# Optimization experiments

Hardware: AMD Instinct MI355X
Metric: run time of the kernel (lower is better)

The kernel has to match this reference:

```python
import jax, jax.numpy as jnp
import numpy as np

B, C_IN, N = 4, 128, 4096
E = 131072           # nnz edges in the sparse adjacency
C_OUT = 128          # module out_channels
C_CONV = C_OUT - 1   # add_counts=True steals one channel for degree counts


def setup_inputs() -> dict:
    key = jax.random.key(0)
    kx, ki, kj, kw, kb = jax.random.split(key, 5)
    x = jax.random.normal(kx, (B, C_IN, N), dtype=jnp.float32)
    # edge list (i, j) for each nonzero of the sparse adjacency
    idx_i = jax.random.randint(ki, (E,), 0, N)
    idx_j = jax.random.randint(kj, (E,), 0, N)
    # Conv1d(in=C_IN, out=C_CONV, kernel_size=2, stride=2) weights
    W = jax.random.normal(kw, (C_CONV, C_IN, 2), dtype=jnp.float32) * 0.05
    b = jax.random.normal(kb, (C_CONV,), dtype=jnp.float32) * 0.05
    return {"x": x, "W": W, "b": b, "idx_i": idx_i, "idx_j": idx_j}


def reference(x, W, b, idx_i, idx_j):
    # _conv: x @ adj_pw.T is a gather of the two endpoints of every edge
    # (adj_pw row 2k selects node idx_i[k], row 2k+1 selects node idx_j[k]).
    # Conv1d(kernel=2, stride=2) then mixes the interleaved endpoint pair:
    #   pair[b,o,e] = sum_c W[o,c,0]*x[b,c,i_e] + W[o,c,1]*x[b,c,j_e] + b[o]
    xi = x[:, :, idx_i]                                   # [B, C, E]
    xj = x[:, :, idx_j]                                   # [B, C, E]
    pair = (jnp.einsum('oc,bce->boe', W[:, :, 0], xi)
            + jnp.einsum('oc,bce->boe', W[:, :, 1], xj)
            + b[None, :, None])                           # [B, C_CONV, E]
    # x @ adj_pw[::2, :] scatter-adds each edge's output to its first endpoint
    n = x.shape[2]
    y = jnp.zeros((x.shape[0], pair.shape[1], n), dtype=x.dtype)
    y = y.at[:, :, idx_i].add(pair)                       # [B, C_CONV, N]
    # adj_sum = adj.to_dense().sum(dim=0): in-degree over columns j
    deg = jnp.zeros((n,), dtype=x.dtype).at[idx_j].add(1.0)
    # normalize: divide by degree clamped to >= 1
    y = y / jnp.where(deg == 0, 1.0, deg)
    # add_counts: append raw degree as an extra channel
    counts = jnp.broadcast_to(deg[None, None, :], (y.shape[0], 1, n))
    return jnp.concatenate([y, counts], axis=1)           # [B, C_OUT, N]
```

## Files before the change

kernel.cpp:

```cpp
#include <hip/hip_runtime.h>
#include <cstdint>
#include <cstddef>

#define BATCH   4
#define CIN     128
#define NN      4096
#define EE      131072
#define CCONV   127
#define NBC     512
#define MAXDEG  128

typedef __attribute__((ext_vector_type(8))) short short8;
typedef __attribute__((ext_vector_type(8))) unsigned short ushort8;
typedef __attribute__((ext_vector_type(4))) float f32x4;

__device__ __forceinline__ unsigned short f2bf(float f) {
    unsigned int u = __float_as_uint(f);
    return (unsigned short)((u + 0x7FFFu + ((u >> 16) & 1u)) >> 16);
}
__device__ __forceinline__ float bf2f(unsigned short h) {
    return __uint_as_float((unsigned int)h << 16);
}

__global__ __launch_bounds__(256) void k_pre(const float* __restrict__ x,
                                             unsigned short* __restrict__ xT,
                                             const float* __restrict__ W,
                                             unsigned short* __restrict__ WTb,
                                             const int* __restrict__ idx_i,
                                             const int* __restrict__ idx_j,
                                             int* __restrict__ cursor,
                                             unsigned short* __restrict__ elist,
                                             int* __restrict__ deg) {
    const int bid = blockIdx.x;
    const int tid = threadIdx.x;
    if (bid < 2048) {
        __shared__ float tile[32][33];
        const int nb = bid & 127;
        const int cb = (bid >> 7) & 3;
        const int b  = bid >> 9;
        const int n0 = nb * 32, c0 = cb * 32;
        const int tx = tid & 31, ty = tid >> 5;
        const float* xb = x + (size_t)b * CIN * NN;
#pragma unroll
        for (int i = 0; i < 4; ++i)
            tile[ty + i * 8][tx] = xb[(size_t)(c0 + ty + i * 8) * NN + n0 + tx];
        __syncthreads();
#pragma unroll
        for (int i = 0; i < 4; ++i) {
            const int nl = ty + i * 8;
            xT[(size_t)(n0 + nl) * NBC + b * CIN + c0 + tx] = f2bf(tile[tx][nl]);
        }
    } else if (bid < 2560) {
        const int e  = (bid - 2048) * 256 + tid;
        const int ni = idx_i[e];
        const int nj = idx_j[e];
        const int pos = atomicAdd(&cursor[ni], 1);
        elist[(size_t)ni * MAXDEG + pos] = (unsigned short)nj;
        atomicAdd(&deg[nj], 1);
    } else {
        const int t = (bid - 2560) * 256 + tid;
        const int o = t >> 8;
        const int k = t & 255;
        float v = 0.0f;
        if (o < CCONV) v = W[((size_t)o * CIN + (k & 127)) * 2 + (k >> 7)];
        WTb[t] = f2bf(v);
    }
}

__global__ __launch_bounds__(256) void k_final(const unsigned short* __restrict__ xT,
                                               const unsigned short* __restrict__ WTb,
                                               const float* __restrict__ bias,
                                               const unsigned short* __restrict__ elist,
                                               const int* __restrict__ cnt_i,
                                               const int* __restrict__ deg,
                                               float* __restrict__ out) {
    __shared__ short Af[1024 * 8];
    __shared__ float cntf[32], invd[32], degf[32], biasf[128];
    __shared__ int   cnti[32];

    const int tid = threadIdx.x;
    const int b   = blockIdx.y;
    const int n0  = blockIdx.x * 32;

    if (tid < 32) {
        const int c = cnt_i[n0 + tid];
        const int d = deg[n0 + tid];
        cnti[tid] = c;
        cntf[tid] = (float)c;
        degf[tid] = (float)d;
        invd[tid] = (d == 0) ? 1.0f : 1.0f / (float)d;
    } else if (tid >= 64 && tid < 192) {
        const int o = tid - 64;
        biasf[o] = (o < CCONV) ? bias[o] : 0.0f;
    }
    __syncthreads();

    const int lane = tid & 63;
    const int w    = tid >> 6;

    {
        const int ns = lane >> 4;
        const int c0 = (lane & 15) * 8;
        const unsigned short* xb = xT + b * CIN + c0;
#pragma unroll
        for (int pg = 0; pg < 2; ++pg) {
            const int j  = w * 8 + pg * 4 + ns;
            const int dn = cnti[j];
            const unsigned short* erow = elist + (size_t)(n0 + j) * MAXDEG;
            float acc[8] = {0, 0, 0, 0, 0, 0, 0, 0};
            int k = 0;
            for (; k + 2 <= dn; k += 2) {
                const int nj0 = erow[k];
                const int nj1 = erow[k + 1];
                const ushort8 u0 = *(const ushort8*)(xb + (size_t)nj0 * NBC);
                const ushort8 u1 = *(const ushort8*)(xb + (size_t)nj1 * NBC);
#pragma unroll
                for (int q = 0; q < 8; ++q) acc[q] += bf2f(u0[q]) + bf2f(u1[q]);
            }
            if (k < dn) {
                const int nj = erow[k];
                const ushort8 u = *(const ushort8*)(xb + (size_t)nj * NBC);
#pragma unroll
                for (int q = 0; q < 8; ++q) acc[q] += bf2f(u[q]);
            }
            short8 p;
#pragma unroll
            for (int q = 0; q < 8; ++q) p[q] = (short)f2bf(acc[q]);
            const int kt   = 4 + (c0 >> 5);
            const int g    = (c0 >> 3) & 3;
            const int unit = ((j >> 4) * 8 + kt) * 64 + (j & 15) + 16 * g;
            *(short8*)&Af[unit * 8] = p;
        }
    }

#pragma unroll
    for (int it = 0; it < 2; ++it) {
        const int u  = tid + it * 256;
        const int L  = u & 63;
        const int kt = (u >> 6) & 3;
        const int mt = u >> 8;
        const int j  = mt * 16 + (L & 15);
        const int k0 = kt * 32 + (L >> 4) * 8;
        const short8 a = *(const short8*)(xT + (size_t)(n0 + j) * NBC + b * CIN + k0);
        const float sc = cntf[j];
        short8 p;
#pragma unroll
        for (int q = 0; q < 8; ++q)
            p[q] = (short)f2bf(bf2f((unsigned short)a[q]) * sc);
        *(short8*)&Af[((mt * 8 + kt) * 64 + L) * 8] = p;
    }
    __syncthreads();

    const int m = lane & 15;
    const int g = lane >> 4;

    f32x4 acc[2][2];
#pragma unroll
    for (int mt = 0; mt < 2; ++mt)
#pragma unroll
        for (int nt = 0; nt < 2; ++nt)
            acc[mt][nt] = (f32x4){0.0f, 0.0f, 0.0f, 0.0f};

    const unsigned short* B0 = WTb + (size_t)(w * 32 + m) * 256;
    const unsigned short* B1 = B0 + 16 * 256;

#pragma unroll
    for (int kt = 0; kt < 8; ++kt) {
        const int k0 = kt * 32 + g * 8;
        const short8 b0 = *(const short8*)(B0 + k0);
        const short8 b1 = *(const short8*)(B1 + k0);
        const short8 a0 = *(const short8*)&Af[((0 * 8 + kt) * 64 + lane) * 8];
        const short8 a1 = *(const short8*)&Af[((1 * 8 + kt) * 64 + lane) * 8];
        acc[0][0] = __builtin_amdgcn_mfma_f32_16x16x32_bf16(a0, b0, acc[0][0], 0, 0, 0);
        acc[0][1] = __builtin_amdgcn_mfma_f32_16x16x32_bf16(a0, b1, acc[0][1], 0, 0, 0);
        acc[1][0] = __builtin_amdgcn_mfma_f32_16x16x32_bf16(a1, b0, acc[1][0], 0, 0, 0);
        acc[1][1] = __builtin_amdgcn_mfma_f32_16x16x32_bf16(a1, b1, acc[1][1], 0, 0, 0);
    }

#pragma unroll
    for (int nt = 0; nt < 2; ++nt) {
        const int o = w * 32 + nt * 16 + m;
        if (o >= CCONV) continue;
        const float bo = biasf[o];
        float* orow = out + ((size_t)b * 128 + o) * NN + n0;
#pragma unroll
        for (int mt = 0; mt < 2; ++mt) {
            const int j0 = mt * 16 + g * 4;
            float4 r;
            r.x = (acc[mt][nt][0] + cntf[j0 + 0] * bo) * invd[j0 + 0];
            r.y = (acc[mt][nt][1] + cntf[j0 + 1] * bo) * invd[j0 + 1];
            r.z = (acc[mt][nt][2] + cntf[j0 + 2] * bo) * invd[j0 + 2];
            r.w = (acc[mt][nt][3] + cntf[j0 + 3] * bo) * invd[j0 + 3];
            *(float4*)(orow + j0) = r;
        }
    }
    if (tid < 32)
        out[((size_t)b * 128 + CCONV) * NN + n0 + tid] = degf[tid];
}

extern "C" void kernel_launch(void* const* d_in, const int* in_sizes, int n_in,
                              void* d_out, int out_size, void* d_ws, size_t ws_size,
                              hipStream_t stream) {
    const float* x    = (const float*)d_in[0];
    const float* W    = (const float*)d_in[1];
    const float* bias = (const float*)d_in[2];
    const int* idx_i  = (const int*)d_in[3];
    const int* idx_j  = (const int*)d_in[4];
    float* out = (float*)d_out;

    char* ws = (char*)d_ws;
    unsigned short* xT     = (unsigned short*)(ws);
    unsigned short* elist  = (unsigned short*)(ws + 4194304);
    unsigned short* WTb    = (unsigned short*)(ws + 5242880);
    int*            cursor = (int*)(ws + 5308416);
    int*            deg    = (int*)(ws + 5324800);

    hipMemsetAsync(cursor, 0, 32768, stream);

    k_pre<<<2688, 256, 0, stream>>>(x, xT, W, WTb, idx_i, idx_j, cursor, elist, deg);
    k_final<<<dim3(NN / 32, BATCH), 256, 0, stream>>>(xT, WTb, bias, elist, cursor, deg, out);
}
```

Baseline: 118.3 us.

## Halve nodes per block, unroll gather by eight, pad atomic counters

Each k_final block now handles 16 nodes instead of 32, which doubles the grid and gives each wave one gather row and one MFMA row-tile. The neighbour gather loads eight edge indices with a single vector load and issues eight row loads before accumulating, to raise memory-level parallelism. The cursor and degree counters are spaced 16 ints apart so that atomics on different nodes fall on separate 64-byte lines, which should reduce contention. In exchange the memset grows to cover the padded counter arrays, and the W tile is reloaded across twice as many blocks.

```diff
diff --git a/kernel.cpp b/kernel.cpp
--- a/kernel.cpp
+++ b/kernel.cpp
@@ -9,6 +9,7 @@
 #define CCONV   127
 #define NBC     512
 #define MAXDEG  128
+#define CPAD    16
 
 typedef __attribute__((ext_vector_type(8))) short short8;
 typedef __attribute__((ext_vector_type(8))) unsigned short ushort8;
@@ -54,9 +55,9 @@
         const int e  = (bid - 2048) * 256 + tid;
         const int ni = idx_i[e];
         const int nj = idx_j[e];
-        const int pos = atomicAdd(&cursor[ni], 1);
+        const int pos = atomicAdd(&cursor[ni * CPAD], 1);
         elist[(size_t)ni * MAXDEG + pos] = (unsigned short)nj;
-        atomicAdd(&deg[nj], 1);
+        atomicAdd(&deg[nj * CPAD], 1);
     } else {
         const int t = (bid - 2560) * 256 + tid;
         const int o = t >> 8;
@@ -74,17 +75,17 @@
                                                const int* __restrict__ cnt_i,
                                                const int* __restrict__ deg,
                                                float* __restrict__ out) {
-    __shared__ short Af[1024 * 8];
-    __shared__ float cntf[32], invd[32], degf[32], biasf[128];
-    __shared__ int   cnti[32];
+    __shared__ short Af[512 * 8];
+    __shared__ float cntf[16], invd[16], degf[16], biasf[128];
+    __shared__ int   cnti[16];
 
     const int tid = threadIdx.x;
     const int b   = blockIdx.y;
-    const int n0  = blockIdx.x * 32;
-
-    if (tid < 32) {
-        const int c = cnt_i[n0 + tid];
-        const int d = deg[n0 + tid];
+    const int n0  = blockIdx.x * 16;
+
+    if (tid < 16) {
+        const int c = cnt_i[(n0 + tid) * CPAD];
+        const int d = deg[(n0 + tid) * CPAD];
         cnti[tid] = c;
         cntf[tid] = (float)c;
         degf[tid] = (float)d;
@@ -100,46 +101,42 @@
 
     {
         const int ns = lane >> 4;
+        const int j  = w * 4 + ns;
         const int c0 = (lane & 15) * 8;
         const unsigned short* xb = xT + b * CIN + c0;
-#pragma unroll
-        for (int pg = 0; pg < 2; ++pg) {
-            const int j  = w * 8 + pg * 4 + ns;
-            const int dn = cnti[j];
-            const unsigned short* erow = elist + (size_t)(n0 + j) * MAXDEG;
-            float acc[8] = {0, 0, 0, 0, 0, 0, 0, 0};
-            int k = 0;
-            for (; k + 2 <= dn; k += 2) {
-                const int nj0 = erow[k];
-                const int nj1 = erow[k + 1];
-                const ushort8 u0 = *(const ushort8*)(xb + (size_t)nj0 * NBC);
-                const ushort8 u1 = *(const ushort8*)(xb + (size_t)nj1 * NBC);
-#pragma unroll
-                for (int q = 0; q < 8; ++q) acc[q] += bf2f(u0[q]) + bf2f(u1[q]);
-            }
-            if (k < dn) {
-                const int nj = erow[k];
-                const ushort8 u = *(const ushort8*)(xb + (size_t)nj * NBC);
-#pragma unroll
-                for (int q = 0; q < 8; ++q) acc[q] += bf2f(u[q]);
-            }
-            short8 p;
-#pragma unroll
-            for (int q = 0; q < 8; ++q) p[q] = (short)f2bf(acc[q]);
-            const int kt   = 4 + (c0 >> 5);
-            const int g    = (c0 >> 3) & 3;
-            const int unit = ((j >> 4) * 8 + kt) * 64 + (j & 15) + 16 * g;
-            *(short8*)&Af[unit * 8] = p;
+        const int dn = cnti[j];
+        const unsigned short* erow = elist + (size_t)(n0 + j) * MAXDEG;
+        float acc[8] = {0, 0, 0, 0, 0, 0, 0, 0};
+        int k = 0;
+        for (; k + 8 <= dn; k += 8) {
+            const ushort8 i8 = *(const ushort8*)(erow + k);
+            ushort8 u[8];
+#pragma unroll
+            for (int t = 0; t < 8; ++t)
+                u[t] = *(const ushort8*)(xb + (size_t)i8[t] * NBC);
+#pragma unroll
+            for (int t = 0; t < 8; ++t)
+#pragma unroll
+                for (int q = 0; q < 8; ++q) acc[q] += bf2f(u[t][q]);
         }
-    }
-
-#pragma unroll
-    for (int it = 0; it < 2; ++it) {
-        const int u  = tid + it * 256;
-        const int L  = u & 63;
-        const int kt = (u >> 6) & 3;
-        const int mt = u >> 8;
-        const int j  = mt * 16 + (L & 15);
+        for (; k < dn; ++k) {
+            const ushort8 u = *(const ushort8*)(xb + (size_t)erow[k] * NBC);
+#pragma unroll
+            for (int q = 0; q < 8; ++q) acc[q] += bf2f(u[q]);
+        }
+        short8 p;
+#pragma unroll
+        for (int q = 0; q < 8; ++q) p[q] = (short)f2bf(acc[q]);
+        const int kt   = 4 + (c0 >> 5);
+        const int g    = (c0 >> 3) & 3;
+        const int unit = kt * 64 + 16 * g + j;
+        *(short8*)&Af[unit * 8] = p;
+    }
+
+    {
+        const int L  = tid & 63;
+        const int kt = tid >> 6;
+        const int j  = L & 15;
         const int k0 = kt * 32 + (L >> 4) * 8;
         const short8 a = *(const short8*)(xT + (size_t)(n0 + j) * NBC + b * CIN + k0);
         const float sc = cntf[j];
@@ -147,19 +144,15 @@
 #pragma unroll
         for (int q = 0; q < 8; ++q)
             p[q] = (short)f2bf(bf2f((unsigned short)a[q]) * sc);
-        *(short8*)&Af[((mt * 8 + kt) * 64 + L) * 8] = p;
+        *(short8*)&Af[(kt * 64 + L) * 8] = p;
     }
     __syncthreads();
 
     const int m = lane & 15;
     const int g = lane >> 4;
 
-    f32x4 acc[2][2];
-#pragma unroll
-    for (int mt = 0; mt < 2; ++mt)
-#pragma unroll
-        for (int nt = 0; nt < 2; ++nt)
-            acc[mt][nt] = (f32x4){0.0f, 0.0f, 0.0f, 0.0f};
+    f32x4 acc0 = (f32x4){0.0f, 0.0f, 0.0f, 0.0f};
+    f32x4 acc1 = (f32x4){0.0f, 0.0f, 0.0f, 0.0f};
 
     const unsigned short* B0 = WTb + (size_t)(w * 32 + m) * 256;
     const unsigned short* B1 = B0 + 16 * 256;
@@ -169,32 +162,27 @@
         const int k0 = kt * 32 + g * 8;
         const short8 b0 = *(const short8*)(B0 + k0);
         const short8 b1 = *(const short8*)(B1 + k0);
-        const short8 a0 = *(const short8*)&Af[((0 * 8 + kt) * 64 + lane) * 8];
-        const short8 a1 = *(const short8*)&Af[((1 * 8 + kt) * 64 + lane) * 8];
-        acc[0][0] = __builtin_amdgcn_mfma_f32_16x16x32_bf16(a0, b0, acc[0][0], 0, 0, 0);
-        acc[0][1] = __builtin_amdgcn_mfma_f32_16x16x32_bf16(a0, b1, acc[0][1], 0, 0, 0);
-        acc[1][0] = __builtin_amdgcn_mfma_f32_16x16x32_bf16(a1, b0, acc[1][0], 0, 0, 0);
-        acc[1][1] = __builtin_amdgcn_mfma_f32_16x16x32_bf16(a1, b1, acc[1][1], 0, 0, 0);
+        const short8 a  = *(const short8*)&Af[(kt * 64 + lane) * 8];
+        acc0 = __builtin_amdgcn_mfma_f32_16x16x32_bf16(a, b0, acc0, 0, 0, 0);
+        acc1 = __builtin_amdgcn_mfma_f32_16x16x32_bf16(a, b1, acc1, 0, 0, 0);
     }
 
 #pragma unroll
     for (int nt = 0; nt < 2; ++nt) {
+        const f32x4 a = nt ? acc1 : acc0;
         const int o = w * 32 + nt * 16 + m;
         if (o >= CCONV) continue;
         const float bo = biasf[o];
         float* orow = out + ((size_t)b * 128 + o) * NN + n0;
-#pragma unroll
-        for (int mt = 0; mt < 2; ++mt) {
-            const int j0 = mt * 16 + g * 4;
-            float4 r;
-            r.x = (acc[mt][nt][0] + cntf[j0 + 0] * bo) * invd[j0 + 0];
-            r.y = (acc[mt][nt][1] + cntf[j0 + 1] * bo) * invd[j0 + 1];
-            r.z = (acc[mt][nt][2] + cntf[j0 + 2] * bo) * invd[j0 + 2];
-            r.w = (acc[mt][nt][3] + cntf[j0 + 3] * bo) * invd[j0 + 3];
-            *(float4*)(orow + j0) = r;
-        }
-    }
-    if (tid < 32)
+        const int j0 = g * 4;
+        float4 r;
+        r.x = (a[0] + cntf[j0 + 0] * bo) * invd[j0 + 0];
+        r.y = (a[1] + cntf[j0 + 1] * bo) * invd[j0 + 1];
+        r.z = (a[2] + cntf[j0 + 2] * bo) * invd[j0 + 2];
+        r.w = (a[3] + cntf[j0 + 3] * bo) * invd[j0 + 3];
+        *(float4*)(orow + j0) = r;
+    }
+    if (tid < 16)
         out[((size_t)b * 128 + CCONV) * NN + n0 + tid] = degf[tid];
 }
 
@@ -213,10 +201,10 @@
     unsigned short* elist  = (unsigned short*)(ws + 4194304);
     unsigned short* WTb    = (unsigned short*)(ws + 5242880);
     int*            cursor = (int*)(ws + 5308416);
-    int*            deg    = (int*)(ws + 5324800);
-
-    hipMemsetAsync(cursor, 0, 32768, stream);
+    int*            deg    = (int*)(ws + 5570560);
+
+    hipMemsetAsync(cursor, 0, 524288, stream);
 
     k_pre<<<2688, 256, 0, stream>>>(x, xT, W, WTb, idx_i, idx_j, cursor, elist, deg);
-    k_final<<<dim3(NN / 32, BATCH), 256, 0, stream>>>(xT, WTb, bias, elist, cursor, deg, out);
-}
+    k_final<<<dim3(NN / 16, BATCH), 256, 0, stream>>>(xT, WTb, bias, elist, cursor, deg, out);
+}
```

Result: faster. 105.2 us (-11.1%).
